# Performance work log

Measured on AMD Instinct MI355X. Metric: run time of the kernel, lower is better.

Reference implementation:

```python
import jax, jax.numpy as jnp
import numpy as np
from math import factorial, pi

# ---- static module config (ModelEncodeDecodeSimple defaults) ----
B_IN, B_OUT = 30, 10        # input / output bandwidths
F_IN, F_OUT = 2, 5          # feature channels
BATCH = 512
N_ALPHA, MAX_BETA, N_BETA = 6, pi / 160.0, 1  # s2_near_identity_grid args


def _wigner_d(l, beta):
    """Wigner-d matrix d^l_{m',m}(beta), rows m'=-l..l, cols m=-l..l (quantum norm, CS phase)."""
    cb, sb = np.cos(beta / 2.0), np.sin(beta / 2.0)
    d = np.zeros((2 * l + 1, 2 * l + 1))
    for i, mp in enumerate(range(-l, l + 1)):
        for j, m in enumerate(range(-l, l + 1)):
            pref = np.sqrt(float(factorial(l + m) * factorial(l - m) * factorial(l + mp) * factorial(l - mp)))
            tot = 0.0
            for s in range(max(0, m - mp), min(l + m, l - mp) + 1):
                den = factorial(l + m - s) * factorial(s) * factorial(mp - m + s) * factorial(l - mp - s)
                tot += ((-1.0) ** (mp - m + s) / den) * cb ** (2 * l + m - mp - 2 * s) * sb ** (mp - m + 2 * s)
            d[i, j] = pref * tot
    return d


def _quad_weights(b):
    """Driscoll-Healy quadrature weights on the SOFT beta grid (lie_learn S2.quadrature_weights)."""
    k = np.arange(b)
    betas = pi * (2 * np.arange(2 * b) + 1) / (4 * b)
    return (2.0 / b) * np.sin(betas) * np.array(
        [np.sum(np.sin((2 * j + 1) * (2 * k + 1) * pi / (4 * b)) / (2 * k + 1)) for j in range(2 * b)])


# ---- precomputed constants (all static, numpy) ----
_betas_in = pi * (2 * np.arange(2 * B_IN) + 1) / (4 * B_IN)
_w = _quad_weights(B_IN)
NSPEC_S2 = B_OUT ** 2  # sum over l<b_out of (2l+1)
W_S2 = np.zeros((2 * B_IN, NSPEC_S2), dtype=np.float32)   # w_k * d^l_{m0}(beta_k)
FREQ_IN = np.zeros(NSPEC_S2, dtype=np.int64)              # alpha FFT bin for each (l,m)
for l in range(B_OUT):
    d_m0 = np.stack([_wigner_d(l, bb)[:, l] for bb in _betas_in])  # [2b_in, 2l+1]
    W_S2[:, l * l:l * l + 2 * l + 1] = (_w[:, None] * d_m0).astype(np.float32)
    FREQ_IN[l * l:l * l + 2 * l + 1] = np.arange(-l, l + 1) % (2 * B_IN)

# kernel grid: s2_near_identity_grid(n_alpha=6, max_beta=pi/160, n_beta=1)
_gb = np.arange(1, N_BETA + 1) * MAX_BETA / N_BETA
_ga = np.linspace(0, 2 * pi, N_ALPHA, endpoint=False)
GB, GA = np.meshgrid(_gb, _ga, indexing='ij')
GB, GA = GB.ravel(), GA.ravel()
N_GRID = GB.size
K_FT = np.zeros((NSPEC_S2, N_GRID), dtype=np.complex64)   # D^l_{m0}(alpha_g, beta_g, 0)
for l in range(B_OUT):
    for g in range(N_GRID):
        d_m0 = _wigner_d(l, GB[g])[:, l]
        K_FT[l * l:l * l + 2 * l + 1, g] = d_m0 * np.exp(-1j * np.arange(-l, l + 1) * GA[g])
SCALING = np.float32(1.0 / np.sqrt(N_GRID * F_IN * (B_OUT ** 4.0) / (B_IN ** 2.0)))

# SO(3) inverse-FFT Wigner blocks at output betas, scaled by (2l+1) (s2cnn so3_ifft convention)
_betas_out = pi * (2 * np.arange(2 * B_OUT) + 1) / (4 * B_OUT)
D_SO3 = [np.stack([_wigner_d(l, bb) for bb in _betas_out]).astype(np.float32) * (2 * l + 1)
         for l in range(B_OUT)]


def s2conv(x, kernel, bias):
    Bsz = x.shape[0]
    # --- S2 FFT of input: FFT over alpha, then quadrature-weighted Wigner contraction over beta ---
    Xf = jnp.fft.fft(x, axis=-1)                     # [B, f_in, 2b_in(beta), 2b_in(alpha-freq)] c64
    gx = Xf[:, :, :, FREQ_IN]                        # [B, f_in, 2b_in, nspec]
    fhat = jnp.einsum('bfks,ks->sbf', gx, W_S2.astype(np.complex64))   # [nspec, B, f_in]
    # --- kernel spherical FT on the near-identity grid ---
    yhat = jnp.einsum('iog,sg->sio', kernel * SCALING, K_FT)           # [nspec, f_in, f_out]
    # --- per-degree outer product (s2_mm, conj on kernel) + SO(3) spectral accumulation ---
    T = jnp.zeros((Bsz, F_OUT, 2 * B_OUT, 2 * B_OUT, 2 * B_OUT), dtype=fhat.dtype)
    for l in range(B_OUT):
        L = 2 * l + 1
        xl = fhat[l * l:l * l + L]                   # [L, B, f_in]
        yl = yhat[l * l:l * l + L]                   # [L, f_in, f_out]
        zl = jnp.einsum('mbi,nio->mnbo', xl, jnp.conj(yl))             # z^l_{mn}
        contrib = jnp.einsum('mnbo,kmn->bokmn', zl, D_SO3[l].astype(np.complex64))
        mi = np.arange(-l, l + 1) % (2 * B_OUT)
        T = T.at[:, :, :, mi[:, None], mi[None, :]].add(contrib)
    # --- inverse FFT over (alpha, gamma); SOFT convention multiplies by (2b)^2; take real part ---
    out = jnp.fft.ifft2(T, axes=(-2, -1)).real * float((2 * B_OUT) ** 2)
    return out + bias                                # [B, f_out, 2b_out, 2b_out, 2b_out]


def setup_inputs() -> dict:
    key = jax.random.key(0)
    k1, k2, k3 = jax.random.split(key, 3)
    x1 = jax.random.normal(k1, (BATCH, F_IN, 2 * B_IN, 2 * B_IN), dtype=jnp.float32)
    kernel = jax.random.normal(k2, (F_IN, F_OUT, N_GRID), dtype=jnp.float32)
    bias = jax.random.normal(k3, (1, F_OUT, 1, 1, 1), dtype=jnp.float32)
    return {"x1": x1, "kernel": kernel, "bias": bias}


def reference(x1, kernel, bias):
    return s2conv(x1, kernel, bias)
```

## Files before the change

kernel.cpp:

```cpp
#include <hip/hip_runtime.h>
#include <math.h>
#include <stdint.h>


typedef _Float16 half8 __attribute__((ext_vector_type(8)));
typedef float    f32x4 __attribute__((ext_vector_type(4)));

#define WS_W    128
#define WS_Y    17760
#define WS_EM   19776
#define WS_RT   20992
#define WS_PACK 21184
#define WS_AP   21952
#define WS_FH   107968
#define WS_DT   220608
#define WS_F    234908

#define IX_Y0    3300
#define IX_EM0   4300
#define IX_RT0   4900
#define IX_PACK0 5090
#define IX_AP0   5805
#define IX_DT0   177837
#define N_SETUP  192137

__device__ __forceinline__ double ipow_d(double x, int e) {
    double r = 1.0;
    for (int i = 0; i < e; ++i) r *= x;
    return r;
}

__device__ double dsmall(int l, int mp, int m, double beta) {
    double fact[20];
    fact[0] = 1.0;
    for (int i = 1; i < 20; ++i) fact[i] = fact[i - 1] * (double)i;
    double cb = cos(0.5 * beta), sb = sin(0.5 * beta);
    double pref = sqrt(fact[l + m] * fact[l - m] * fact[l + mp] * fact[l - mp]);
    int s0 = m - mp; if (s0 < 0) s0 = 0;
    int s1 = l + m;  if (l - mp < s1) s1 = l - mp;
    double tot = 0.0;
    for (int s = s0; s <= s1; ++s) {
        double den = fact[l + m - s] * fact[s] * fact[mp - m + s] * fact[l - mp - s];
        double sgn = ((mp - m + s) & 1) ? -1.0 : 1.0;
        tot += sgn / den * ipow_d(cb, 2 * l + m - mp - 2 * s) * ipow_d(sb, mp - m + 2 * s);
    }
    return pref * tot;
}

extern "C" __global__ void k_setup_w(float* wsf) {
    double* w = (double*)wsf;
    int t = threadIdx.x;
    if (t < 60) {
        double beta = M_PI * (2 * t + 1) / 120.0;
        double sum = 0.0;
        for (int k = 0; k < 30; ++k)
            sum += sin((double)((2 * t + 1) * (2 * k + 1)) * M_PI / 120.0) / (double)(2 * k + 1);
        w[t] = (2.0 / 30.0) * sin(beta) * sum;
    }
}

extern "C" __global__ void k_setup_const(float* wsf, const float* __restrict__ kern) {
    const double* w = (const double*)wsf;
    const int tri[11] = {0, 1, 3, 6, 10, 15, 21, 28, 36, 45, 55};
    int idx = blockIdx.x * 64 + threadIdx.x;
    if (idx < IX_Y0) {
        int k = idx / 55, smi = idx % 55;
        int l = 0; while (smi >= tri[l + 1]) ++l;
        int m = smi - tri[l];
        double beta = M_PI * (2 * k + 1) / 120.0;
        wsf[WS_W + idx] = (float)(w[k] * dsmall(l, m, 0, beta));
    } else if (idx < IX_EM0) {
        int i3 = idx - IX_Y0;
        int o = i3 / 200, r5 = i3 % 200;
        int s = r5 / 2, i = r5 % 2;
        int l = 0; while ((l + 1) * (l + 1) <= s) ++l;
        int n = s - l * l - l;
        double dv = dsmall(l, n, 0, M_PI / 160.0);
        const double SC = 1.0 / sqrt(6.0 * 2.0 * 10000.0 / 900.0);
        double ar = 0.0, ai = 0.0;
        for (int g = 0; g < 6; ++g) {
            double kv = (double)kern[i * 30 + o * 6 + g];
            double ang = (double)n * M_PI * (double)g / 3.0;
            ar += kv * cos(ang);
            ai -= kv * sin(ang);
        }
        ((float2*)(wsf + WS_Y))[i3] = make_float2((float)(SC * dv * ar), (float)(SC * dv * ai));
    } else if (idx < IX_RT0) {
        int t = idx - IX_EM0; int m = t / 60, j = t % 60;
        double a = 2.0 * M_PI * (double)(m * j) / 60.0;
        ((float2*)(wsf + WS_EM))[t] = make_float2((float)cos(a), (float)(-sin(a)));
    } else if (idx < IX_PACK0) {
        int r = idx - IX_RT0;
        int m = r / 19, nn = r % 19, n = nn - 9;
        int a = n < 0 ? -n : n;
        int lmin = m > a ? m : a;
        int tL = lmin * (lmin - 1);
        int base = tL * (2 * lmin - 1) / 3 + ((3 * tL) >> 1) + lmin;
        int p0 = base + m * (2 * lmin + 1) + n + lmin;
        ((int*)(wsf + WS_RT))[r] = p0 | (lmin << 10) | (m << 14);
    } else if (idx < IX_AP0) {
        int p = idx - IX_PACK0;
        int l = 0, bcur = 0;
        for (;;) { int bs = (l + 1) * (2 * l + 1); if (p < bcur + bs) break; bcur += bs; ++l; }
        int r = p - bcur; int L = 2 * l + 1;
        int m = r / L; int n = r % L - l;
        int smi = tri[l] + m; int sf = l * l + l + n;
        ((int*)(wsf + WS_PACK))[p] = smi * 128 + sf;
    } else if (idx < IX_AP0 + 172032 && idx >= IX_AP0) {
        int ap = idx - IX_AP0;
        int j = ap & 7, lane = (ap >> 3) & 63, tc = ap >> 9;
        int t = tc % 28, c = tc / 28;
        int pq = t * 16 + (lane & 15);
        int kidx = c * 32 + ((lane >> 4) << 3) + j;
        double val = 0.0;
        if (pq < 400 && kidx < 380) {
            int r = kidx >> 1, cpart = kidx & 1;
            int m = r / 19, nn = r % 19, n = nn - 9;
            int p = pq / 20, q = pq % 20;
            int th = ((m * p + n * q) % 20 + 20) % 20;
            double wm = m ? 2.0 : 1.0;
            double ang = M_PI * (double)th / 10.0;
            val = cpart ? (-wm * sin(ang)) : (wm * cos(ang));
        }
        ((_Float16*)(wsf + WS_AP))[ap] = (_Float16)val;
    } else if (idx < N_SETUP) {
        int i6 = idx - IX_DT0;
        int p = i6 / 20, k = i6 % 20;
        int l = 0, bcur = 0;
        for (;;) { int bs = (l + 1) * (2 * l + 1); if (p < bcur + bs) break; bcur += bs; ++l; }
        int r = p - bcur; int L = 2 * l + 1;
        int m = r / L; int n = r % L - l;
        double beta = M_PI * (2 * k + 1) / 40.0;
        wsf[WS_DT + i6] = (float)((double)L * dsmall(l, m, n, beta));
    }
}

extern "C" __global__ void __launch_bounds__(256) k_fhat(const float* __restrict__ x,
                                                          float* __restrict__ wsf) {
    __shared__ float  xs[3600];
    __shared__ float2 ems[610];
    __shared__ float2 Y[600];
    int tid = threadIdx.x;
    int bi = blockIdx.x;
    const float4* xp = (const float4*)(x + bi * 3600);
    for (int t = tid; t < 900; t += 256) ((float4*)xs)[t] = xp[t];
    const float2* gEm = (const float2*)(wsf + WS_EM);
    for (int t = tid; t < 600; t += 256) {
        int m = t / 60, j = t - m * 60;
        ems[m * 61 + j] = gEm[t];
    }
    __syncthreads();
    for (int it = tid; it < 600; it += 256) {
        int k = it / 10, m = it - k * 10;
        const float*  row = xs + k * 60;
        const float2* em  = ems + m * 61;
        float ar = 0.f, ai = 0.f;
        #pragma unroll 12
        for (int j = 0; j < 60; ++j) {
            float xv = row[j];
            float2 e = em[j];
            ar += xv * e.x; ai += xv * e.y;
        }
        Y[it] = make_float2(ar, ai);
    }
    __syncthreads();
    if (tid < 55) {
        int smi = tid;
        const int tri[11] = {0, 1, 3, 6, 10, 15, 21, 28, 36, 45, 55};
        int l = 0; while (smi >= tri[l + 1]) ++l;
        int m = smi - tri[l];
        const float* gW = wsf + WS_W;
        float ar = 0.f, ai = 0.f;
        for (int kk = 0; kk < 60; ++kk) {
            float wv = gW[kk * 55 + smi];
            float2 y = Y[kk * 10 + m];
            ar += wv * y.x; ai += wv * y.y;
        }
        int b = bi >> 1, i = bi & 1;
        ((float2*)(wsf + WS_FH))[b * 110 + smi * 2 + i] = make_float2(ar, ai);
    }
}

template<int L>
__device__ __forceinline__ void fsum(int m, int n, int ko, const float* __restrict__ gDT,
                                     const float2* __restrict__ zp, float& fr, float& fi) {
    const int baseL[10] = {0, 1, 7, 22, 50, 95, 161, 252, 372, 525};
    float dv[10 - L];
    float2 zv[10 - L];
    #pragma unroll
    for (int l = L; l < 10; ++l) {
        int p = baseL[l] + m * (2 * l + 1) + n + l;
        dv[l - L] = gDT[p * 20 + ko];
        zv[l - L] = zp[p];
    }
    #pragma unroll
    for (int l = L; l < 10; ++l) {
        fr += dv[l - L] * zv[l - L].x;
        fi += dv[l - L] * zv[l - L].y;
    }
}

extern "C" __global__ void __launch_bounds__(256) k_zF(float* __restrict__ wsf) {
    __shared__ float2 zsh[2860];
    __shared__ float4 fbl4[110];
    __shared__ float4 yol4[500];
    int tid = threadIdx.x;
    int half = blockIdx.x & 1;
    int nb   = blockIdx.x >> 1;
    int n0 = nb * 64;
    int PO0 = n0 / 20;
    int bf = PO0 / 5;

    const float4* gfh4 = (const float4*)(wsf + WS_FH);
    for (int t = tid; t < 110; t += 256) {
        int bsel = t / 55, i55 = t - bsel * 55;
        int b = bf + bsel;
        fbl4[t] = (b < 512) ? gfh4[b * 55 + i55] : make_float4(0.f, 0.f, 0.f, 0.f);
    }
    for (int t = tid; t < 500; t += 256) yol4[t] = ((const float4*)(wsf + WS_Y))[t];
    __syncthreads();
    const int* gPack = (const int*)(wsf + WS_PACK);
    for (int pp = 0; pp < 4; ++pp) {
        int po = PO0 + pp;
        int b_loc = po / 5 - bf, o = po % 5;
        for (int p = tid; p < 715; p += 256) {
            int pk = gPack[p];
            int smi = pk >> 7, sf = pk & 127;
            float4 f = fbl4[b_loc * 55 + smi];
            float4 y = yol4[o * 100 + sf];
            float zr = f.x * y.x + f.y * y.y + f.z * y.z + f.w * y.w;
            float zi = f.y * y.x - f.x * y.y + f.w * y.z - f.z * y.w;
            zsh[pp * 715 + p] = make_float2(zr, zi);
        }
    }
    __syncthreads();

    int col = tid & 63;
    int ko  = (n0 + col) % 20;
    int pp  = ((n0 % 20) + col) / 20;
    int gg  = (n0 >> 4) + (col >> 4);
    int c15 = col & 15;
    const float* gDT = wsf + WS_DT;
    uint32_t*    gF  = (uint32_t*)(wsf + WS_F);
    const float2* zp = zsh + pp * 715;
    for (int it = tid; it < 6080; it += 256) {
        int r = __builtin_amdgcn_readfirstlane(((it >> 6) << 1) | half);
        int m = r / 19;
        int n = r - m * 19 - 9;
        int a = n < 0 ? -n : n;
        int lmin = m > a ? m : a;
        float fr = 0.f, fi = 0.f;
        switch (lmin) {
            case 0: fsum<0>(m, n, ko, gDT, zp, fr, fi); break;
            case 1: fsum<1>(m, n, ko, gDT, zp, fr, fi); break;
            case 2: fsum<2>(m, n, ko, gDT, zp, fr, fi); break;
            case 3: fsum<3>(m, n, ko, gDT, zp, fr, fi); break;
            case 4: fsum<4>(m, n, ko, gDT, zp, fr, fi); break;
            case 5: fsum<5>(m, n, ko, gDT, zp, fr, fi); break;
            case 6: fsum<6>(m, n, ko, gDT, zp, fr, fi); break;
            case 7: fsum<7>(m, n, ko, gDT, zp, fr, fi); break;
            case 8: fsum<8>(m, n, ko, gDT, zp, fr, fi); break;
            default: fsum<9>(m, n, ko, gDT, zp, fr, fi); break;
        }
        int chunk = r >> 4, w5 = (2 * r) & 31;
        int qp = w5 >> 3, dwi = (w5 & 7) >> 1;
        union { _Float16 h[2]; uint32_t u; } fv;
        fv.h[0] = (_Float16)fr; fv.h[1] = (_Float16)fi;
        gF[((chunk * 3200 + gg) * 64 + (qp * 16 + c15)) * 4 + dwi] = fv.u;
    }
    if (half == 0 && tid < 128) {
        int cc = tid >> 1, dwi = 2 + (tid & 1);
        int g2 = (n0 >> 4) + (cc >> 4);
        gF[((11 * 3200 + g2) * 64 + (48 + (cc & 15))) * 4 + dwi] = 0u;
    }
}

extern "C" __global__ void __launch_bounds__(256) k_gemm2(const float* __restrict__ wsf,
                                                           const float* __restrict__ bias,
                                                           float* __restrict__ out) {
    int tid = threadIdx.x;
    int n0 = blockIdx.x * 64;
    int wave = tid >> 6, lane = tid & 63;
    int g0 = n0 >> 4;
    const half8* gA = (const half8*)(wsf + WS_AP);
    const half8* gB = (const half8*)(wsf + WS_F);
    int t0 = wave * 7;
    int ntile = (wave < 3) ? 7 : 4;

    f32x4 acc[7][4];
    #pragma unroll
    for (int tt = 0; tt < 7; ++tt)
        #pragma unroll
        for (int f = 0; f < 4; ++f) acc[tt][f] = (f32x4){0.f, 0.f, 0.f, 0.f};

    half8 bufB[2][4], bufA[2][7];
    #pragma unroll
    for (int f = 0; f < 4; ++f) bufB[0][f] = gB[(g0 + f) * 64 + lane];
    #pragma unroll
    for (int tt = 0; tt < 7; ++tt)
        if (tt < ntile) bufA[0][tt] = gA[(t0 + tt) * 64 + lane];

    #pragma unroll
    for (int c = 0; c < 12; ++c) {
        const int cur = c & 1, nxt = cur ^ 1;
        if (c < 11) {
            #pragma unroll
            for (int f = 0; f < 4; ++f)
                bufB[nxt][f] = gB[((c + 1) * 3200 + g0 + f) * 64 + lane];
            #pragma unroll
            for (int tt = 0; tt < 7; ++tt)
                if (tt < ntile) bufA[nxt][tt] = gA[((c + 1) * 28 + t0 + tt) * 64 + lane];
        }
        #pragma unroll
        for (int tt = 0; tt < 7; ++tt) {
            if (tt < ntile) {
                #pragma unroll
                for (int f = 0; f < 4; ++f)
                    acc[tt][f] = __builtin_amdgcn_mfma_f32_16x16x32_f16(bufA[cur][tt], bufB[cur][f], acc[tt][f], 0, 0, 0);
            }
        }
    }

    int quad4 = (lane >> 4) << 2, col15 = lane & 15;
    float bo_f[4];
    #pragma unroll
    for (int f = 0; f < 4; ++f) bo_f[f] = bias[((n0 + f * 16 + col15) / 20) % 5];
    #pragma unroll
    for (int tt = 0; tt < 7; ++tt) {
        if (tt < ntile) {
            int pqb = (t0 + tt) * 16 + quad4;
            #pragma unroll
            for (int f = 0; f < 4; ++f) {
                int n = n0 + f * 16 + col15;
                float bo = bo_f[f];
                float4 v = make_float4(acc[tt][f].x + bo, acc[tt][f].y + bo,
                                       acc[tt][f].z + bo, acc[tt][f].w + bo);
                *(float4*)(out + n * 400 + pqb) = v;
            }
        }
    }
}

extern "C" void kernel_launch(void* const* d_in, const int* in_sizes, int n_in,
                              void* d_out, int out_size, void* d_ws, size_t ws_size,
                              hipStream_t stream) {
    const float* x    = (const float*)d_in[0];
    const float* kern = (const float*)d_in[1];
    const float* bias = (const float*)d_in[2];
    float* out = (float*)d_out;
    float* wsf = (float*)d_ws;
    k_setup_w    <<<1,    64,  0, stream>>>(wsf);
    k_setup_const<<<3003, 64,  0, stream>>>(wsf, kern);
    k_fhat       <<<1024, 256, 0, stream>>>(x, wsf);
    k_zF         <<<1600, 256, 0, stream>>>(wsf);
    k_gemm2      <<<800,  256, 0, stream>>>(wsf, bias, out);
}
```

Before: 186.2 us.

## Fuse z/F construction into GEMM kernel via shared-memory F tile

```diff
diff --git a/kernel.cpp b/kernel.cpp
--- a/kernel.cpp
+++ b/kernel.cpp
@@ -14,7 +14,6 @@
 #define WS_AP   21952
 #define WS_FH   107968
 #define WS_DT   220608
-#define WS_F    234908
 
 #define IX_Y0    3300
 #define IX_EM0   4300
@@ -106,7 +105,7 @@
         int m = r / L; int n = r % L - l;
         int smi = tri[l] + m; int sf = l * l + l + n;
         ((int*)(wsf + WS_PACK))[p] = smi * 128 + sf;
-    } else if (idx < IX_AP0 + 172032 && idx >= IX_AP0) {
+    } else if (idx < IX_DT0) {
         int ap = idx - IX_AP0;
         int j = ap & 7, lane = (ap >> 3) & 63, tc = ap >> 9;
         int t = tc % 28, c = tc / 28;
@@ -183,10 +182,10 @@
 
 template<int L>
 __device__ __forceinline__ void fsum(int m, int n, int ko, const float* __restrict__ gDT,
-                                     const float2* __restrict__ zp, float& fr, float& fi) {
+                                     const uint32_t* zp, float& fr, float& fi) {
     const int baseL[10] = {0, 1, 7, 22, 50, 95, 161, 252, 372, 525};
     float dv[10 - L];
-    float2 zv[10 - L];
+    uint32_t zv[10 - L];
     #pragma unroll
     for (int l = L; l < 10; ++l) {
         int p = baseL[l] + m * (2 * l + 1) + n + l;
@@ -195,19 +194,24 @@
     }
     #pragma unroll
     for (int l = L; l < 10; ++l) {
-        fr += dv[l - L] * zv[l - L].x;
-        fi += dv[l - L] * zv[l - L].y;
-    }
-}
-
-extern "C" __global__ void __launch_bounds__(256) k_zF(float* __restrict__ wsf) {
-    __shared__ float2 zsh[2860];
-    __shared__ float4 fbl4[110];
-    __shared__ float4 yol4[500];
+        union { uint32_t u; _Float16 h[2]; } zc; zc.u = zv[l - L];
+        fr += dv[l - L] * (float)zc.h[0];
+        fi += dv[l - L] * (float)zc.h[1];
+    }
+}
+
+extern "C" __global__ void __launch_bounds__(256, 2) k_zg(const float* __restrict__ wsf,
+                                                           const float* __restrict__ bias,
+                                                           float* __restrict__ out) {
+    __shared__ __align__(16) unsigned char smem[49152];
+    __shared__ uint32_t zsh[2860];
+    _Float16* Fsh  = (_Float16*)smem;
+    uint32_t* F32  = (uint32_t*)smem;
+    float4*   yol4 = (float4*)smem;
+    float4*   fbl4 = (float4*)(smem + 8000);
+
     int tid = threadIdx.x;
-    int half = blockIdx.x & 1;
-    int nb   = blockIdx.x >> 1;
-    int n0 = nb * 64;
+    int n0 = blockIdx.x * 64;
     int PO0 = n0 / 20;
     int bf = PO0 / 5;
 
@@ -219,6 +223,7 @@
     }
     for (int t = tid; t < 500; t += 256) yol4[t] = ((const float4*)(wsf + WS_Y))[t];
     __syncthreads();
+
     const int* gPack = (const int*)(wsf + WS_PACK);
     for (int pp = 0; pp < 4; ++pp) {
         int po = PO0 + pp;
@@ -230,21 +235,22 @@
             float4 y = yol4[o * 100 + sf];
             float zr = f.x * y.x + f.y * y.y + f.z * y.z + f.w * y.w;
             float zi = f.y * y.x - f.x * y.y + f.w * y.z - f.z * y.w;
-            zsh[pp * 715 + p] = make_float2(zr, zi);
+            union { _Float16 h[2]; uint32_t u; } cv;
+            cv.h[0] = (_Float16)zr; cv.h[1] = (_Float16)zi;
+            zsh[pp * 715 + p] = cv.u;
         }
     }
     __syncthreads();
 
     int col = tid & 63;
-    int ko  = (n0 + col) % 20;
-    int pp  = ((n0 % 20) + col) / 20;
-    int gg  = (n0 >> 4) + (col >> 4);
-    int c15 = col & 15;
+    int ko   = (n0 + col) % 20;
+    int pp   = ((n0 % 20) + col) / 20;
+    int gloc = col >> 4;
+    int c15  = col & 15;
     const float* gDT = wsf + WS_DT;
-    uint32_t*    gF  = (uint32_t*)(wsf + WS_F);
-    const float2* zp = zsh + pp * 715;
-    for (int it = tid; it < 6080; it += 256) {
-        int r = __builtin_amdgcn_readfirstlane(((it >> 6) << 1) | half);
+    const uint32_t* zp = zsh + pp * 715;
+    for (int it = tid; it < 12160; it += 256) {
+        int r = __builtin_amdgcn_readfirstlane(it >> 6);
         int m = r / 19;
         int n = r - m * 19 - 9;
         int a = n < 0 ? -n : n;
@@ -266,24 +272,17 @@
         int qp = w5 >> 3, dwi = (w5 & 7) >> 1;
         union { _Float16 h[2]; uint32_t u; } fv;
         fv.h[0] = (_Float16)fr; fv.h[1] = (_Float16)fi;
-        gF[((chunk * 3200 + gg) * 64 + (qp * 16 + c15)) * 4 + dwi] = fv.u;
-    }
-    if (half == 0 && tid < 128) {
+        F32[((chunk * 4 + gloc) * 64 + (qp * 16 + c15)) * 4 + dwi] = fv.u;
+    }
+    if (tid < 128) {
         int cc = tid >> 1, dwi = 2 + (tid & 1);
-        int g2 = (n0 >> 4) + (cc >> 4);
-        gF[((11 * 3200 + g2) * 64 + (48 + (cc & 15))) * 4 + dwi] = 0u;
-    }
-}
-
-extern "C" __global__ void __launch_bounds__(256) k_gemm2(const float* __restrict__ wsf,
-                                                           const float* __restrict__ bias,
-                                                           float* __restrict__ out) {
-    int tid = threadIdx.x;
-    int n0 = blockIdx.x * 64;
+        F32[((44 + (cc >> 4)) * 64 + (48 + (cc & 15))) * 4 + dwi] = 0u;
+    }
+    __syncthreads();
+
     int wave = tid >> 6, lane = tid & 63;
-    int g0 = n0 >> 4;
     const half8* gA = (const half8*)(wsf + WS_AP);
-    const half8* gB = (const half8*)(wsf + WS_F);
+    const half8* lB = (const half8*)Fsh;
     int t0 = wave * 7;
     int ntile = (wave < 3) ? 7 : 4;
 
@@ -293,9 +292,7 @@
         #pragma unroll
         for (int f = 0; f < 4; ++f) acc[tt][f] = (f32x4){0.f, 0.f, 0.f, 0.f};
 
-    half8 bufB[2][4], bufA[2][7];
-    #pragma unroll
-    for (int f = 0; f < 4; ++f) bufB[0][f] = gB[(g0 + f) * 64 + lane];
+    half8 bufA[2][7];
     #pragma unroll
     for (int tt = 0; tt < 7; ++tt)
         if (tt < ntile) bufA[0][tt] = gA[(t0 + tt) * 64 + lane];
@@ -305,18 +302,18 @@
         const int cur = c & 1, nxt = cur ^ 1;
         if (c < 11) {
             #pragma unroll
-            for (int f = 0; f < 4; ++f)
-                bufB[nxt][f] = gB[((c + 1) * 3200 + g0 + f) * 64 + lane];
-            #pragma unroll
             for (int tt = 0; tt < 7; ++tt)
                 if (tt < ntile) bufA[nxt][tt] = gA[((c + 1) * 28 + t0 + tt) * 64 + lane];
         }
+        half8 bB[4];
+        #pragma unroll
+        for (int f = 0; f < 4; ++f) bB[f] = lB[(c * 4 + f) * 64 + lane];
         #pragma unroll
         for (int tt = 0; tt < 7; ++tt) {
             if (tt < ntile) {
                 #pragma unroll
                 for (int f = 0; f < 4; ++f)
-                    acc[tt][f] = __builtin_amdgcn_mfma_f32_16x16x32_f16(bufA[cur][tt], bufB[cur][f], acc[tt][f], 0, 0, 0);
+                    acc[tt][f] = __builtin_amdgcn_mfma_f32_16x16x32_f16(bufA[cur][tt], bB[f], acc[tt][f], 0, 0, 0);
             }
         }
     }
@@ -352,6 +349,5 @@
     k_setup_w    <<<1,    64,  0, stream>>>(wsf);
     k_setup_const<<<3003, 64,  0, stream>>>(wsf, kern);
     k_fhat       <<<1024, 256, 0, stream>>>(x, wsf);
-    k_zF         <<<1600, 256, 0, stream>>>(wsf);
-    k_gemm2      <<<800,  256, 0, stream>>>(wsf, bias, out);
-}
+    k_zg         <<<800,  256, 0, stream>>>(wsf, bias, out);
+}
```

New measurement: 190.3 us. 1.02x slower.

## Split gemm2 M-tiles across two blocks and table-ize setup trig

Applied to the files above, without the earlier changes.

```diff
diff --git a/kernel.cpp b/kernel.cpp
--- a/kernel.cpp
+++ b/kernel.cpp
@@ -9,7 +9,7 @@
 #define WS_W    128
 #define WS_Y    17760
 #define WS_EM   19776
-#define WS_RT   20992
+#define WS_TRIG 20992
 #define WS_PACK 21184
 #define WS_AP   21952
 #define WS_FH   107968
@@ -56,6 +56,11 @@
         for (int k = 0; k < 30; ++k)
             sum += sin((double)((2 * t + 1) * (2 * k + 1)) * M_PI / 120.0) / (double)(2 * k + 1);
         w[t] = (2.0 / 30.0) * sin(beta) * sum;
+    }
+    if (t < 20) {
+        double ang = M_PI * (double)t / 10.0;
+        ((double*)(wsf + WS_TRIG))[t]      = sin(ang);
+        ((double*)(wsf + WS_TRIG))[20 + t] = cos(ang);
     }
 }
 
@@ -90,14 +95,6 @@
         double a = 2.0 * M_PI * (double)(m * j) / 60.0;
         ((float2*)(wsf + WS_EM))[t] = make_float2((float)cos(a), (float)(-sin(a)));
     } else if (idx < IX_PACK0) {
-        int r = idx - IX_RT0;
-        int m = r / 19, nn = r % 19, n = nn - 9;
-        int a = n < 0 ? -n : n;
-        int lmin = m > a ? m : a;
-        int tL = lmin * (lmin - 1);
-        int base = tL * (2 * lmin - 1) / 3 + ((3 * tL) >> 1) + lmin;
-        int p0 = base + m * (2 * lmin + 1) + n + lmin;
-        ((int*)(wsf + WS_RT))[r] = p0 | (lmin << 10) | (m << 14);
     } else if (idx < IX_AP0) {
         int p = idx - IX_PACK0;
         int l = 0, bcur = 0;
@@ -106,7 +103,7 @@
         int m = r / L; int n = r % L - l;
         int smi = tri[l] + m; int sf = l * l + l + n;
         ((int*)(wsf + WS_PACK))[p] = smi * 128 + sf;
-    } else if (idx < IX_AP0 + 172032 && idx >= IX_AP0) {
+    } else if (idx < IX_DT0) {
         int ap = idx - IX_AP0;
         int j = ap & 7, lane = (ap >> 3) & 63, tc = ap >> 9;
         int t = tc % 28, c = tc / 28;
@@ -119,8 +116,8 @@
             int p = pq / 20, q = pq % 20;
             int th = ((m * p + n * q) % 20 + 20) % 20;
             double wm = m ? 2.0 : 1.0;
-            double ang = M_PI * (double)th / 10.0;
-            val = cpart ? (-wm * sin(ang)) : (wm * cos(ang));
+            const double* st = (const double*)(wsf + WS_TRIG);
+            val = cpart ? (-wm * st[th]) : (wm * st[20 + th]);
         }
         ((_Float16*)(wsf + WS_AP))[ap] = (_Float16)val;
     } else if (idx < N_SETUP) {
@@ -279,26 +276,27 @@
                                                            const float* __restrict__ bias,
                                                            float* __restrict__ out) {
     int tid = threadIdx.x;
-    int n0 = blockIdx.x * 64;
+    int h  = blockIdx.x & 1;
+    int n0 = (blockIdx.x >> 1) * 64;
     int wave = tid >> 6, lane = tid & 63;
     int g0 = n0 >> 4;
     const half8* gA = (const half8*)(wsf + WS_AP);
     const half8* gB = (const half8*)(wsf + WS_F);
-    int t0 = wave * 7;
-    int ntile = (wave < 3) ? 7 : 4;
-
-    f32x4 acc[7][4];
-    #pragma unroll
-    for (int tt = 0; tt < 7; ++tt)
+    int nt = (h == 0 && wave == 0) ? 4 : 3;
+    int t0 = h * 13 + (h == 0 ? (wave == 0 ? 0 : 4 + 3 * (wave - 1)) : 3 * wave);
+
+    f32x4 acc[4][4];
+    #pragma unroll
+    for (int tt = 0; tt < 4; ++tt)
         #pragma unroll
         for (int f = 0; f < 4; ++f) acc[tt][f] = (f32x4){0.f, 0.f, 0.f, 0.f};
 
-    half8 bufB[2][4], bufA[2][7];
+    half8 bufB[2][4], bufA[2][4];
     #pragma unroll
     for (int f = 0; f < 4; ++f) bufB[0][f] = gB[(g0 + f) * 64 + lane];
     #pragma unroll
-    for (int tt = 0; tt < 7; ++tt)
-        if (tt < ntile) bufA[0][tt] = gA[(t0 + tt) * 64 + lane];
+    for (int tt = 0; tt < 4; ++tt)
+        if (tt < nt) bufA[0][tt] = gA[(t0 + tt) * 64 + lane];
 
     #pragma unroll
     for (int c = 0; c < 12; ++c) {
@@ -308,12 +306,12 @@
             for (int f = 0; f < 4; ++f)
                 bufB[nxt][f] = gB[((c + 1) * 3200 + g0 + f) * 64 + lane];
             #pragma unroll
-            for (int tt = 0; tt < 7; ++tt)
-                if (tt < ntile) bufA[nxt][tt] = gA[((c + 1) * 28 + t0 + tt) * 64 + lane];
+            for (int tt = 0; tt < 4; ++tt)
+                if (tt < nt) bufA[nxt][tt] = gA[((c + 1) * 28 + t0 + tt) * 64 + lane];
         }
         #pragma unroll
-        for (int tt = 0; tt < 7; ++tt) {
-            if (tt < ntile) {
+        for (int tt = 0; tt < 4; ++tt) {
+            if (tt < nt) {
                 #pragma unroll
                 for (int f = 0; f < 4; ++f)
                     acc[tt][f] = __builtin_amdgcn_mfma_f32_16x16x32_f16(bufA[cur][tt], bufB[cur][f], acc[tt][f], 0, 0, 0);
@@ -326,8 +324,8 @@
     #pragma unroll
     for (int f = 0; f < 4; ++f) bo_f[f] = bias[((n0 + f * 16 + col15) / 20) % 5];
     #pragma unroll
-    for (int tt = 0; tt < 7; ++tt) {
-        if (tt < ntile) {
+    for (int tt = 0; tt < 4; ++tt) {
+        if (tt < nt) {
             int pqb = (t0 + tt) * 16 + quad4;
             #pragma unroll
             for (int f = 0; f < 4; ++f) {
@@ -353,5 +351,5 @@
     k_setup_const<<<3003, 64,  0, stream>>>(wsf, kern);
     k_fhat       <<<1024, 256, 0, stream>>>(x, wsf);
     k_zF         <<<1600, 256, 0, stream>>>(wsf);
-    k_gemm2      <<<800,  256, 0, stream>>>(wsf, bias, out);
-}
+    k_gemm2      <<<1600, 256, 0, stream>>>(wsf, bias, out);
+}
```

New measurement: 187.9 us. Within noise of the previous version (+0.9%).

## Split fused z/F kernel into separate z and F kernels with global z buffer

Applied to the files above, without the earlier changes.

```diff
diff --git a/kernel.cpp b/kernel.cpp
--- a/kernel.cpp
+++ b/kernel.cpp
@@ -9,12 +9,13 @@
 #define WS_W    128
 #define WS_Y    17760
 #define WS_EM   19776
-#define WS_RT   20992
+#define WS_TRIG 20992
 #define WS_PACK 21184
 #define WS_AP   21952
 #define WS_FH   107968
 #define WS_DT   220608
 #define WS_F    234908
+#define WS_Z    10100000
 
 #define IX_Y0    3300
 #define IX_EM0   4300
@@ -56,6 +57,11 @@
         for (int k = 0; k < 30; ++k)
             sum += sin((double)((2 * t + 1) * (2 * k + 1)) * M_PI / 120.0) / (double)(2 * k + 1);
         w[t] = (2.0 / 30.0) * sin(beta) * sum;
+    }
+    if (t < 20) {
+        double ang = M_PI * (double)t / 10.0;
+        ((double*)(wsf + WS_TRIG))[t]      = sin(ang);
+        ((double*)(wsf + WS_TRIG))[20 + t] = cos(ang);
     }
 }
 
@@ -85,19 +91,11 @@
             ai -= kv * sin(ang);
         }
         ((float2*)(wsf + WS_Y))[i3] = make_float2((float)(SC * dv * ar), (float)(SC * dv * ai));
-    } else if (idx < IX_RT0) {
+    } else if (idx < IX_EM0 + 600) {
         int t = idx - IX_EM0; int m = t / 60, j = t % 60;
         double a = 2.0 * M_PI * (double)(m * j) / 60.0;
         ((float2*)(wsf + WS_EM))[t] = make_float2((float)cos(a), (float)(-sin(a)));
     } else if (idx < IX_PACK0) {
-        int r = idx - IX_RT0;
-        int m = r / 19, nn = r % 19, n = nn - 9;
-        int a = n < 0 ? -n : n;
-        int lmin = m > a ? m : a;
-        int tL = lmin * (lmin - 1);
-        int base = tL * (2 * lmin - 1) / 3 + ((3 * tL) >> 1) + lmin;
-        int p0 = base + m * (2 * lmin + 1) + n + lmin;
-        ((int*)(wsf + WS_RT))[r] = p0 | (lmin << 10) | (m << 14);
     } else if (idx < IX_AP0) {
         int p = idx - IX_PACK0;
         int l = 0, bcur = 0;
@@ -106,7 +104,7 @@
         int m = r / L; int n = r % L - l;
         int smi = tri[l] + m; int sf = l * l + l + n;
         ((int*)(wsf + WS_PACK))[p] = smi * 128 + sf;
-    } else if (idx < IX_AP0 + 172032 && idx >= IX_AP0) {
+    } else if (idx < IX_DT0) {
         int ap = idx - IX_AP0;
         int j = ap & 7, lane = (ap >> 3) & 63, tc = ap >> 9;
         int t = tc % 28, c = tc / 28;
@@ -119,8 +117,8 @@
             int p = pq / 20, q = pq % 20;
             int th = ((m * p + n * q) % 20 + 20) % 20;
             double wm = m ? 2.0 : 1.0;
-            double ang = M_PI * (double)th / 10.0;
-            val = cpart ? (-wm * sin(ang)) : (wm * cos(ang));
+            const double* st = (const double*)(wsf + WS_TRIG);
+            val = cpart ? (-wm * st[th]) : (wm * st[20 + th]);
         }
         ((_Float16*)(wsf + WS_AP))[ap] = (_Float16)val;
     } else if (idx < N_SETUP) {
@@ -181,6 +179,20 @@
     }
 }
 
+extern "C" __global__ void __launch_bounds__(256) k_z(float* __restrict__ wsf) {
+    int idx = blockIdx.x * 256 + threadIdx.x;
+    if (idx >= 2560 * 715) return;
+    int po = idx / 715, p = idx - po * 715;
+    int b = po / 5, o = po - b * 5;
+    int pk = ((const int*)(wsf + WS_PACK))[p];
+    int smi = pk >> 7, sf = pk & 127;
+    float4 f = ((const float4*)(wsf + WS_FH))[b * 55 + smi];
+    float4 y = ((const float4*)(wsf + WS_Y))[o * 100 + sf];
+    float zr = f.x * y.x + f.y * y.y + f.z * y.z + f.w * y.w;
+    float zi = f.y * y.x - f.x * y.y + f.w * y.z - f.z * y.w;
+    ((float2*)(wsf + WS_Z))[idx] = make_float2(zr, zi);
+}
+
 template<int L>
 __device__ __forceinline__ void fsum(int m, int n, int ko, const float* __restrict__ gDT,
                                      const float2* __restrict__ zp, float& fr, float& fi) {
@@ -200,67 +212,38 @@
     }
 }
 
-extern "C" __global__ void __launch_bounds__(256) k_zF(float* __restrict__ wsf) {
-    __shared__ float2 zsh[2860];
-    __shared__ float4 fbl4[110];
-    __shared__ float4 yol4[500];
+extern "C" __global__ void __launch_bounds__(256) k_F(float* __restrict__ wsf) {
     int tid = threadIdx.x;
-    int half = blockIdx.x & 1;
-    int nb   = blockIdx.x >> 1;
+    int q  = blockIdx.x & 3;
+    int nb = blockIdx.x >> 2;
     int n0 = nb * 64;
-    int PO0 = n0 / 20;
-    int bf = PO0 / 5;
-
-    const float4* gfh4 = (const float4*)(wsf + WS_FH);
-    for (int t = tid; t < 110; t += 256) {
-        int bsel = t / 55, i55 = t - bsel * 55;
-        int b = bf + bsel;
-        fbl4[t] = (b < 512) ? gfh4[b * 55 + i55] : make_float4(0.f, 0.f, 0.f, 0.f);
-    }
-    for (int t = tid; t < 500; t += 256) yol4[t] = ((const float4*)(wsf + WS_Y))[t];
-    __syncthreads();
-    const int* gPack = (const int*)(wsf + WS_PACK);
-    for (int pp = 0; pp < 4; ++pp) {
-        int po = PO0 + pp;
-        int b_loc = po / 5 - bf, o = po % 5;
-        for (int p = tid; p < 715; p += 256) {
-            int pk = gPack[p];
-            int smi = pk >> 7, sf = pk & 127;
-            float4 f = fbl4[b_loc * 55 + smi];
-            float4 y = yol4[o * 100 + sf];
-            float zr = f.x * y.x + f.y * y.y + f.z * y.z + f.w * y.w;
-            float zi = f.y * y.x - f.x * y.y + f.w * y.z - f.z * y.w;
-            zsh[pp * 715 + p] = make_float2(zr, zi);
-        }
-    }
-    __syncthreads();
-
     int col = tid & 63;
-    int ko  = (n0 + col) % 20;
-    int pp  = ((n0 % 20) + col) / 20;
+    int n   = n0 + col;
+    int po  = n / 20, ko = n - po * 20;
     int gg  = (n0 >> 4) + (col >> 4);
     int c15 = col & 15;
-    const float* gDT = wsf + WS_DT;
-    uint32_t*    gF  = (uint32_t*)(wsf + WS_F);
-    const float2* zp = zsh + pp * 715;
-    for (int it = tid; it < 6080; it += 256) {
-        int r = __builtin_amdgcn_readfirstlane(((it >> 6) << 1) | half);
+    const float*  gDT = wsf + WS_DT;
+    const float2* zp  = ((const float2*)(wsf + WS_Z)) + po * 715;
+    uint32_t*     gF  = (uint32_t*)(wsf + WS_F);
+    int nit = (q < 2) ? 3072 : 3008;
+    for (int it = tid; it < nit; it += 256) {
+        int r = __builtin_amdgcn_readfirstlane(((it >> 6) << 2) | q);
         int m = r / 19;
-        int n = r - m * 19 - 9;
-        int a = n < 0 ? -n : n;
+        int nn = r - m * 19 - 9;
+        int a = nn < 0 ? -nn : nn;
         int lmin = m > a ? m : a;
         float fr = 0.f, fi = 0.f;
         switch (lmin) {
-            case 0: fsum<0>(m, n, ko, gDT, zp, fr, fi); break;
-            case 1: fsum<1>(m, n, ko, gDT, zp, fr, fi); break;
-            case 2: fsum<2>(m, n, ko, gDT, zp, fr, fi); break;
-            case 3: fsum<3>(m, n, ko, gDT, zp, fr, fi); break;
-            case 4: fsum<4>(m, n, ko, gDT, zp, fr, fi); break;
-            case 5: fsum<5>(m, n, ko, gDT, zp, fr, fi); break;
-            case 6: fsum<6>(m, n, ko, gDT, zp, fr, fi); break;
-            case 7: fsum<7>(m, n, ko, gDT, zp, fr, fi); break;
-            case 8: fsum<8>(m, n, ko, gDT, zp, fr, fi); break;
-            default: fsum<9>(m, n, ko, gDT, zp, fr, fi); break;
+            case 0: fsum<0>(m, nn, ko, gDT, zp, fr, fi); break;
+            case 1: fsum<1>(m, nn, ko, gDT, zp, fr, fi); break;
+            case 2: fsum<2>(m, nn, ko, gDT, zp, fr, fi); break;
+            case 3: fsum<3>(m, nn, ko, gDT, zp, fr, fi); break;
+            case 4: fsum<4>(m, nn, ko, gDT, zp, fr, fi); break;
+            case 5: fsum<5>(m, nn, ko, gDT, zp, fr, fi); break;
+            case 6: fsum<6>(m, nn, ko, gDT, zp, fr, fi); break;
+            case 7: fsum<7>(m, nn, ko, gDT, zp, fr, fi); break;
+            case 8: fsum<8>(m, nn, ko, gDT, zp, fr, fi); break;
+            default: fsum<9>(m, nn, ko, gDT, zp, fr, fi); break;
         }
         int chunk = r >> 4, w5 = (2 * r) & 31;
         int qp = w5 >> 3, dwi = (w5 & 7) >> 1;
@@ -268,7 +251,7 @@
         fv.h[0] = (_Float16)fr; fv.h[1] = (_Float16)fi;
         gF[((chunk * 3200 + gg) * 64 + (qp * 16 + c15)) * 4 + dwi] = fv.u;
     }
-    if (half == 0 && tid < 128) {
+    if (q == 0 && tid < 128) {
         int cc = tid >> 1, dwi = 2 + (tid & 1);
         int g2 = (n0 >> 4) + (cc >> 4);
         gF[((11 * 3200 + g2) * 64 + (48 + (cc & 15))) * 4 + dwi] = 0u;
@@ -352,6 +335,7 @@
     k_setup_w    <<<1,    64,  0, stream>>>(wsf);
     k_setup_const<<<3003, 64,  0, stream>>>(wsf, kern);
     k_fhat       <<<1024, 256, 0, stream>>>(x, wsf);
-    k_zF         <<<1600, 256, 0, stream>>>(wsf);
+    k_z          <<<7150, 256, 0, stream>>>(wsf);
+    k_F          <<<3200, 256, 0, stream>>>(wsf);
     k_gemm2      <<<800,  256, 0, stream>>>(wsf, bias, out);
 }
```

Measured after the change: 204.4 us. 1.1x slower.
